# Performance work log

Measured on AMD Instinct MI355X. Metric: run time of the kernel, lower is better.

## Reference

```python
import jax, jax.numpy as jnp
import numpy as np

B, HW, ENC = 64, 14, 2048
L, V, E, D, A = 20, 10000, 512, 512, 512
T = L - 1  # max decode length (one caption forced to length L)


def setup_inputs() -> dict:
    key = jax.random.key(0)
    ks = jax.random.split(key, 16)

    def p(k, shape, s=0.02):
        return jax.random.normal(k, shape, jnp.float32) * s

    cl = jax.random.randint(ks[2], (B,), 5, L + 1).at[0].set(L)
    return {
        "encoder_out": jax.random.normal(ks[0], (B, HW, HW, ENC), jnp.float32),
        "encoded_captions": jax.random.randint(ks[1], (B, L), 0, V),
        "caption_lengths": cl[:, None].astype(jnp.int32),
        "emb": jax.random.uniform(ks[3], (V, E), jnp.float32, -0.1, 0.1),
        "W_ih": p(ks[4], (4 * D, E + ENC)), "b_ih": jnp.zeros((4 * D,), jnp.float32),
        "W_hh": p(ks[5], (4 * D, D)), "b_hh": jnp.zeros((4 * D,), jnp.float32),
        "W_init_h": p(ks[6], (D, ENC)), "b_init_h": jnp.zeros((D,), jnp.float32),
        "W_init_c": p(ks[7], (D, ENC)), "b_init_c": jnp.zeros((D,), jnp.float32),
        "W_fbeta": p(ks[8], (ENC, D)), "b_fbeta": jnp.zeros((ENC,), jnp.float32),
        "W_fc": jax.random.uniform(ks[9], (V, D), jnp.float32, -0.1, 0.1), "b_fc": jnp.zeros((V,), jnp.float32),
        "W_enc_att": p(ks[10], (A, ENC)), "b_enc_att": jnp.zeros((A,), jnp.float32),
        "W_dec_att": p(ks[11], (A, D)), "b_dec_att": jnp.zeros((A,), jnp.float32),
        "W_full_att": p(ks[12], (1, A)), "b_full_att": jnp.zeros((1,), jnp.float32),
    }


def _decode(encoder_out, encoded_captions, caption_lengths, emb,
            W_ih, b_ih, W_hh, b_hh, W_init_h, b_init_h, W_init_c, b_init_c,
            W_fbeta, b_fbeta, W_fc, b_fc, W_enc_att, b_enc_att,
            W_dec_att, b_dec_att, W_full_att, b_full_att):
    b = encoder_out.shape[0]
    enc = encoder_out.reshape(b, -1, encoder_out.shape[-1])  # [B, P, ENC]
    cl = caption_lengths[:, 0]
    sort_ind = jnp.argsort(-cl)  # descending by caption length
    cl = cl[sort_ind]
    enc = enc[sort_ind]
    caps = encoded_captions[sort_ind]
    decode_lengths = cl - 1  # per-sample number of decode steps

    mean_enc = jnp.mean(enc, axis=1)  # [B, ENC]
    h0 = mean_enc @ W_init_h.T + b_init_h
    c0 = mean_enc @ W_init_c.T + b_init_c

    embeddings = emb[caps]  # [B, L, E]
    # encoder-side attention projection is h-independent: precompute once
    att1 = jnp.einsum('bpe,ae->bpa', enc, W_enc_att) + b_enc_att  # [B, P, A]

    xs_emb = jnp.swapaxes(embeddings[:, :T], 0, 1)  # [T, B, E]
    masks = decode_lengths[None, :] > jnp.arange(T)[:, None]  # [T, B]
    # Note: torch slices h[:batch_size_t]; since batch is length-sorted descending,
    # masking inactive rows (freeze state, zero outputs) computes identical values.

    def step(carry, xs):
        h, c = carry
        emb_t, mask = xs
        # Bahdanau soft attention
        att2 = h @ W_dec_att.T + b_dec_att  # [B, A]
        e = jnp.einsum('bpa,a->bp', jnp.tanh(att1 + att2[:, None, :]), W_full_att[0]) + b_full_att[0]
        alpha = jax.nn.softmax(e, axis=1)  # [B, P]
        awe = jnp.einsum('bp,bpe->be', alpha, enc)  # [B, ENC]
        gate = jax.nn.sigmoid(h @ W_fbeta.T + b_fbeta)
        x = jnp.concatenate([emb_t, gate * awe], axis=1)  # [B, E+ENC]
        # LSTMCell (torch gate order: i, f, g, o)
        gates = x @ W_ih.T + b_ih + h @ W_hh.T + b_hh
        i, f, g, o = jnp.split(gates, 4, axis=1)
        c_new = jax.nn.sigmoid(f) * c + jax.nn.sigmoid(i) * jnp.tanh(g)
        h_new = jax.nn.sigmoid(o) * jnp.tanh(c_new)
        preds = h_new @ W_fc.T + b_fc  # dropout = identity in eval
        m = mask[:, None]
        h = jnp.where(m, h_new, h)
        c = jnp.where(m, c_new, c)
        return (h, c), (jnp.where(m, preds, 0.0), jnp.where(m, alpha, 0.0))

    (_, _), (preds, alphas) = jax.lax.scan(step, (h0, c0), (xs_emb, masks))
    predictions = jnp.swapaxes(preds, 0, 1)  # [B, T, V]
    alphas = jnp.swapaxes(alphas, 0, 1)      # [B, T, P]
    return predictions, caps, alphas, sort_ind


def reference(encoder_out, encoded_captions, caption_lengths, emb,
              W_ih, b_ih, W_hh, b_hh, W_init_h, b_init_h, W_init_c, b_init_c,
              W_fbeta, b_fbeta, W_fc, b_fc, W_enc_att, b_enc_att,
              W_dec_att, b_dec_att, W_full_att, b_full_att):
    return _decode(encoder_out, encoded_captions, caption_lengths, emb,
                   W_ih, b_ih, W_hh, b_hh, W_init_h, b_init_h, W_init_c, b_init_c,
                   W_fbeta, b_fbeta, W_fc, b_fc, W_enc_att, b_enc_att,
                   W_dec_att, b_dec_att, W_full_att, b_full_att)
```

## Files before the change

### kernel.cpp

```cpp
#include <hip/hip_runtime.h>
#include <math.h>

#define Bb 64
#define Pp 196
#define ENCd 2048
#define Lc 20
#define Tt 19
#define Vv 10000
#define Ee 512
#define Dd 512
#define Aa 512
#define K2 2560
#define KG 3072
#define G4 2048
#define NPAD 10112

#define OUT_PRED 0ll
#define OUT_CAPS 12160000ll
#define OUT_ALPH 12161280ll
#define OUT_SIND 12399616ll

typedef unsigned short ushort_t;
typedef __attribute__((ext_vector_type(8))) short short8;
typedef __attribute__((ext_vector_type(4))) float f32x4;

#define MFMA16 __builtin_amdgcn_mfma_f32_16x16x32_bf16

__device__ __forceinline__ float b2f(ushort_t u) {
    union { unsigned int i; float f; } x; x.i = ((unsigned int)u) << 16; return x.f;
}
__device__ __forceinline__ ushort_t f2b(float f) {
    union { float f; unsigned int i; } x; x.f = f;
    unsigned int r = x.i + 0x7fffu + ((x.i >> 16) & 1u);
    return (ushort_t)(r >> 16);
}
__device__ __forceinline__ float fsig(float x) { return 1.0f / (1.0f + __expf(-x)); }
__device__ __forceinline__ float ftanh(float x) {
    x = fminf(fmaxf(x, -15.0f), 15.0f);
    float e = __expf(2.0f * x);
    return (e - 1.0f) / (e + 1.0f);
}

__global__ void k_sort(const int* __restrict__ cap_len, const int* __restrict__ caps_in,
                       float* __restrict__ out, int* __restrict__ sind,
                       int* __restrict__ dlen, int* __restrict__ caps_s) {
    __shared__ int cls[Bb];
    int i = threadIdx.x;
    int cl = cap_len[i];
    cls[i] = cl;
    __syncthreads();
    int rank = 0;
    for (int j = 0; j < Bb; ++j) {
        int cj = cls[j];
        rank += (cj > cl) || (cj == cl && j < i);
    }
    sind[rank] = i;
    dlen[rank] = cl - 1;
    out[OUT_SIND + rank] = (float)i;
    for (int l = 0; l < Lc; ++l) {
        int v = caps_in[i * Lc + l];
        caps_s[rank * Lc + l] = v;
        out[OUT_CAPS + rank * Lc + l] = (float)v;
    }
}

__device__ __forceinline__ void cvtseg(const float* __restrict__ src, ushort_t* __restrict__ dst,
                                       int cols, int stride, int off, int bid0, long long quads) {
    long long qid = (long long)bid0 * 256 + threadIdx.x;
    if (qid >= quads) return;
    int c4pr = cols >> 2;
    int r = (int)(qid / c4pr), c4 = (int)(qid % c4pr) << 2;
    float4 v = *(const float4*)&src[(size_t)r * cols + c4];
    ushort4 o; o.x = f2b(v.x); o.y = f2b(v.y); o.z = f2b(v.z); o.w = f2b(v.w);
    *(ushort4*)&dst[(size_t)r * stride + off + c4] = o;
}

__global__ void k_cvtall(const float* Wdec, const float* Wfb, const float* Wih,
                         const float* Whh, const float* Wfc, const float* Wenc_f,
                         const float* Wih0, const float* Wic0,
                         ushort_t* W_ag, ushort_t* W_cat, ushort_t* W_fcb,
                         ushort_t* W_enc, ushort_t* W_hcb) {
    int b = blockIdx.x;
    if      (b < 256)   cvtseg(Wdec,  W_ag,               512,  512,  0,    b,         65536);
    else if (b < 1280)  cvtseg(Wfb,   W_ag + 512 * 512,   512,  512,  0,    b - 256,   262144);
    else if (b < 6400)  cvtseg(Wih,   W_cat,              2560, 3072, 0,    b - 1280,  1310720);
    else if (b < 7424)  cvtseg(Whh,   W_cat,              512,  3072, 2560, b - 6400,  262144);
    else if (b < 12424) cvtseg(Wfc,   W_fcb,              512,  512,  0,    b - 7424,  1280000);
    else if (b < 13448) cvtseg(Wenc_f,W_enc,              2048, 2048, 0,    b - 12424, 262144);
    else if (b < 14472) cvtseg(Wih0,  W_hcb,              2048, 2048, 0,    b - 13448, 262144);
    else                cvtseg(Wic0,  W_hcb + 512 * 2048, 2048, 2048, 0,    b - 14472, 262144);
}

__global__ void k_bias(const float* b_dec, const float* b_fb, const float* b_ihp,
                       const float* b_hhp, const float* b_h, const float* b_c,
                       float* b_ag, float* bsum, float* b_hc) {
    int id = blockIdx.x * 256 + threadIdx.x;
    if (id < 512) b_ag[id] = b_dec[id];
    else if (id < 2560) b_ag[id] = b_fb[id - 512];
    if (id < 2048) bsum[id] = b_ihp[id] + b_hhp[id];
    if (id < 512) b_hc[id] = b_h[id];
    else if (id < 1024) b_hc[id] = b_c[id - 512];
}

__global__ void __launch_bounds__(256) k_enccvt(const float* __restrict__ enc,
                                                const int* __restrict__ sind,
                                                ushort_t* __restrict__ enc_bf) {
    const long long total8 = (long long)Bb * Pp * ENCd / 8;
    for (long long u = (long long)blockIdx.x * 256 + threadIdx.x; u < total8;
         u += (long long)gridDim.x * 256) {
        long long flat = u * 8;
        int r = (int)(flat >> 11);
        int c8 = (int)(flat & 2047);
        int b = r / Pp;
        size_t srow = (size_t)sind[b] * Pp + (r - b * Pp);
        const float* s = enc + srow * ENCd + c8;
        float4 v0 = *(const float4*)s;
        float4 v1 = *(const float4*)(s + 4);
        short8 o;
        o[0] = (short)f2b(v0.x); o[1] = (short)f2b(v0.y); o[2] = (short)f2b(v0.z); o[3] = (short)f2b(v0.w);
        o[4] = (short)f2b(v1.x); o[5] = (short)f2b(v1.y); o[6] = (short)f2b(v1.z); o[7] = (short)f2b(v1.w);
        *(short8*)&enc_bf[(size_t)r * ENCd + c8] = o;
    }
}

__global__ void __launch_bounds__(1024) k_meanenc(const ushort_t* __restrict__ enc_bf,
                                                  ushort_t* __restrict__ mean_bf) {
    int b = blockIdx.x;
    int lane = threadIdx.x & 63, w = threadIdx.x >> 6;
    int cg = w & 3, pg = w >> 2;
    int lc = cg * 512 + lane * 8;
    __shared__ float red[4][2048];
    float acc[8] = {};
    for (int p = pg; p < Pp; p += 4) {
        short8 v = *(const short8*)&enc_bf[((size_t)b * Pp + p) * ENCd + lc];
        #pragma unroll
        for (int j = 0; j < 8; ++j) acc[j] += b2f((ushort_t)v[j]);
    }
    #pragma unroll
    for (int j = 0; j < 8; ++j) red[pg][lc + j] = acc[j];
    __syncthreads();
    int tid = threadIdx.x;
    float2 s = {0.f, 0.f};
    #pragma unroll
    for (int g = 0; g < 4; ++g) {
        float2 v = *(const float2*)&red[g][tid * 2];
        s.x += v.x; s.y += v.y;
    }
    ushort2 o; o.x = f2b(s.x * (1.0f / Pp)); o.y = f2b(s.y * (1.0f / Pp));
    *(ushort2*)&mean_bf[(size_t)b * ENCd + tid * 2] = o;
}

__global__ void __launch_bounds__(256) k_att1(const ushort_t* __restrict__ enc_bf,
                                              const ushort_t* __restrict__ Wenc,
                                              const float* __restrict__ benc,
                                              ushort_t* __restrict__ att1) {
    __shared__ ushort_t As[128 * 64];
    __shared__ ushort_t Bs[128 * 64];
    int tid = threadIdx.x;
    int lane = tid & 63, w = tid >> 6;
    int wr = w >> 1, wc = w & 1;
    int d = blockIdx.x;
    int lid = (d & 7) * 49 + (d >> 3);
    int by = lid >> 2, bx = lid & 3;
    int m0 = by * 128, n0 = bx * 128;
    int r16 = lane & 15;
    f32x4 acc[4][4];
    #pragma unroll
    for (int mf = 0; mf < 4; ++mf)
        #pragma unroll
        for (int nf = 0; nf < 4; ++nf) acc[mf][nf] = (f32x4){0.f, 0.f, 0.f, 0.f};

    int lrow = lane >> 3;
    int lslot = lane & 7;
    for (int k0 = 0; k0 < ENCd; k0 += 64) {
        __syncthreads();
        #pragma unroll
        for (int c = 0; c < 4; ++c) {
            int row = c * 32 + w * 8 + lrow;
            int kg = lslot ^ (row & 7);
            const ushort_t* asrc = enc_bf + (size_t)(m0 + row) * ENCd + k0 + kg * 8;
            const ushort_t* bsrc = Wenc   + (size_t)(n0 + row) * ENCd + k0 + kg * 8;
            __builtin_amdgcn_global_load_lds(
                (const __attribute__((address_space(1))) void*)asrc,
                (__attribute__((address_space(3))) void*)&As[(c * 32 + w * 8) * 64], 16, 0, 0);
            __builtin_amdgcn_global_load_lds(
                (const __attribute__((address_space(1))) void*)bsrc,
                (__attribute__((address_space(3))) void*)&Bs[(c * 32 + w * 8) * 64], 16, 0, 0);
        }
        __syncthreads();
        #pragma unroll
        for (int ks = 0; ks < 2; ++ks) {
            int sl = ks * 4 + (lane >> 4);
            short8 a[4], b[4];
            #pragma unroll
            for (int mf = 0; mf < 4; ++mf) {
                int row = wr * 64 + mf * 16 + r16;
                a[mf] = *(const short8*)&As[row * 64 + ((sl ^ (row & 7)) << 3)];
            }
            #pragma unroll
            for (int nf = 0; nf < 4; ++nf) {
                int row = wc * 64 + nf * 16 + r16;
                b[nf] = *(const short8*)&Bs[row * 64 + ((sl ^ (row & 7)) << 3)];
            }
            #pragma unroll
            for (int mf = 0; mf < 4; ++mf)
                #pragma unroll
                for (int nf = 0; nf < 4; ++nf)
                    acc[mf][nf] = MFMA16(a[mf], b[nf], acc[mf][nf], 0, 0, 0);
        }
    }
    int rj0 = (lane >> 4) << 2;
    #pragma unroll
    for (int mf = 0; mf < 4; ++mf)
        #pragma unroll
        for (int nf = 0; nf < 4; ++nf) {
            int col = n0 + wc * 64 + nf * 16 + r16;
            float bv = benc[col];
            #pragma unroll
            for (int j = 0; j < 4; ++j) {
                int row = m0 + wr * 64 + mf * 16 + rj0 + j;
                att1[(size_t)row * Aa + col] = f2b(acc[mf][nf][j] + bv);
            }
        }
}

__global__ void __launch_bounds__(256) k_h0c0(
        const ushort_t* __restrict__ A, const ushort_t* __restrict__ W,
        const float* __restrict__ bias, ushort_t* __restrict__ hout,
        float* __restrict__ cst) {
    int lane = threadIdx.x & 63, w = threadIdx.x >> 6;
    int r16 = lane & 15, kq = (lane >> 4) << 3;
    int ncol[4];
    #pragma unroll
    for (int tt = 0; tt < 4; ++tt) ncol[tt] = blockIdx.x * 64 + tt * 16 + r16;
    f32x4 acc[4][4];
    #pragma unroll
    for (int mt = 0; mt < 4; ++mt)
        #pragma unroll
        for (int tt = 0; tt < 4; ++tt) acc[mt][tt] = (f32x4){0.f, 0.f, 0.f, 0.f};
    for (int k0 = w * 512; k0 < w * 512 + 512; k0 += 32) {
        short8 a[4];
        #pragma unroll
        for (int mt = 0; mt < 4; ++mt)
            a[mt] = *(const short8*)(A + (size_t)(mt * 16 + r16) * ENCd + k0 + kq);
        #pragma unroll
        for (int tt = 0; tt < 4; ++tt) {
            short8 bw = *(const short8*)&W[(size_t)ncol[tt] * ENCd + k0 + kq];
            #pragma unroll
            for (int mt = 0; mt < 4; ++mt)
                acc[mt][tt] = MFMA16(a[mt], bw, acc[mt][tt], 0, 0, 0);
        }
    }
    __shared__ float red[2][64][68];
    if (w >= 2) {
        float* row = &red[w - 2][lane][0];
        #pragma unroll
        for (int mt = 0; mt < 4; ++mt)
            #pragma unroll
            for (int tt = 0; tt < 4; ++tt) *(f32x4*)&row[(mt * 4 + tt) * 4] = acc[mt][tt];
    }
    __syncthreads();
    if (w < 2) {
        float* row = &red[w][lane][0];
        #pragma unroll
        for (int mt = 0; mt < 4; ++mt)
            #pragma unroll
            for (int tt = 0; tt < 4; ++tt) acc[mt][tt] += *(f32x4*)&row[(mt * 4 + tt) * 4];
    }
    __syncthreads();
    if (w == 1) {
        float* row = &red[0][lane][0];
        #pragma unroll
        for (int mt = 0; mt < 4; ++mt)
            #pragma unroll
            for (int tt = 0; tt < 4; ++tt) *(f32x4*)&row[(mt * 4 + tt) * 4] = acc[mt][tt];
    }
    __syncthreads();
    if (w != 0) return;
    {
        float* row = &red[0][lane][0];
        #pragma unroll
        for (int mt = 0; mt < 4; ++mt)
            #pragma unroll
            for (int tt = 0; tt < 4; ++tt) acc[mt][tt] += *(f32x4*)&row[(mt * 4 + tt) * 4];
    }
    int rj0 = (lane >> 4) << 2;
    #pragma unroll
    for (int mt = 0; mt < 4; ++mt)
        #pragma unroll
        for (int tt = 0; tt < 4; ++tt) {
            int col = ncol[tt];
            float bv = bias[col];
            #pragma unroll
            for (int j = 0; j < 4; ++j) {
                int row = mt * 16 + rj0 + j;
                float v = acc[mt][tt][j] + bv;
                if (col < 512) hout[row * Dd + col] = f2b(v);
                else           cst[row * Dd + (col - 512)] = v;
            }
        }
}

__global__ void __launch_bounds__(256) k_ag(
        const ushort_t* __restrict__ h, const ushort_t* __restrict__ W,
        const float* __restrict__ bias, float* __restrict__ of) {
    int lane = threadIdx.x & 63, w = threadIdx.x >> 6;
    int r16 = lane & 15, kq = (lane >> 4) << 3;
    int col = blockIdx.x * 16 + r16;
    f32x4 acc[4];
    #pragma unroll
    for (int mt = 0; mt < 4; ++mt) acc[mt] = (f32x4){0.f, 0.f, 0.f, 0.f};
    for (int k0 = w * 128; k0 < w * 128 + 128; k0 += 32) {
        short8 bw = *(const short8*)&W[(size_t)col * Dd + k0 + kq];
        #pragma unroll
        for (int mt = 0; mt < 4; ++mt) {
            short8 a = *(const short8*)(h + (size_t)(mt * 16 + r16) * Dd + k0 + kq);
            acc[mt] = MFMA16(a, bw, acc[mt], 0, 0, 0);
        }
    }
    __shared__ float red[2][64][20];
    if (w >= 2) {
        float* rr = &red[w - 2][lane][0];
        #pragma unroll
        for (int mt = 0; mt < 4; ++mt) *(f32x4*)&rr[mt * 4] = acc[mt];
    }
    __syncthreads();
    if (w < 2) {
        float* rr = &red[w][lane][0];
        #pragma unroll
        for (int mt = 0; mt < 4; ++mt) acc[mt] += *(f32x4*)&rr[mt * 4];
    }
    __syncthreads();
    if (w == 1) {
        float* rr = &red[0][lane][0];
        #pragma unroll
        for (int mt = 0; mt < 4; ++mt) *(f32x4*)&rr[mt * 4] = acc[mt];
    }
    __syncthreads();
    if (w != 0) return;
    {
        float* rr = &red[0][lane][0];
        #pragma unroll
        for (int mt = 0; mt < 4; ++mt) acc[mt] += *(f32x4*)&rr[mt * 4];
    }
    int rj0 = (lane >> 4) << 2;
    float bv = bias[col];
    #pragma unroll
    for (int mt = 0; mt < 4; ++mt)
        #pragma unroll
        for (int j = 0; j < 4; ++j) {
            int row = mt * 16 + rj0 + j;
            float v = acc[mt][j] + bv;
            of[(size_t)row * K2 + col] = (col >= 512) ? fsig(v) : v;
        }
}

__global__ void __launch_bounds__(1024) k_esmawe(
        const ushort_t* __restrict__ att1, const float* __restrict__ ag,
        const float* __restrict__ wfull, const float* __restrict__ bfull,
        const ushort_t* __restrict__ enc_bf,
        const float* __restrict__ emb, const int* __restrict__ caps_s,
        ushort_t* __restrict__ x2, float* __restrict__ out,
        const int* __restrict__ dlen, int t) {
    int b = blockIdx.x >> 2, ch = blockIdx.x & 3;
    int tid = threadIdx.x;
    int lane = tid & 63, wv = tid >> 6;
    __shared__ float att2f[512], wfl[512];
    __shared__ float e_sh[200], al_sh[200], sm[4];
    __shared__ float redA[16][512];
    if (tid < 512) att2f[tid] = ag[(size_t)b * K2 + tid];
    else           wfl[tid - 512] = wfull[tid - 512];
    __syncthreads();
    float a2[8], wf8[8];
    #pragma unroll
    for (int j = 0; j < 8; ++j) { a2[j] = att2f[lane * 8 + j]; wf8[j] = wfl[lane * 8 + j]; }
    float bf0 = bfull[0];
    for (int p0 = wv; p0 < Pp; p0 += 32) {
        int p1 = p0 + 16;
        bool has1 = p1 < Pp;
        short8 v0 = *(const short8*)&att1[((size_t)b * Pp + p0) * Aa + lane * 8];
        short8 v1 = has1 ? *(const short8*)&att1[((size_t)b * Pp + p1) * Aa + lane * 8] : v0;
        float s0 = 0.f, s1 = 0.f;
        #pragma unroll
        for (int j = 0; j < 8; ++j) {
            s0 += ftanh(b2f((ushort_t)v0[j]) + a2[j]) * wf8[j];
            s1 += ftanh(b2f((ushort_t)v1[j]) + a2[j]) * wf8[j];
        }
        #pragma unroll
        for (int o = 32; o; o >>= 1) {
            s0 += __shfl_xor(s0, o);
            s1 += __shfl_xor(s1, o);
        }
        if (lane == 0) {
            e_sh[p0] = s0 + bf0;
            if (has1) e_sh[p1] = s1 + bf0;
        }
    }
    __syncthreads();
    if (wv == 0) {
        float v0 = e_sh[lane];
        float v1 = e_sh[lane + 64];
        float v2 = e_sh[lane + 128];
        float v3 = (lane + 192 < Pp) ? e_sh[lane + 192] : -1e30f;
        float m = fmaxf(fmaxf(v0, v1), fmaxf(v2, v3));
        #pragma unroll
        for (int o = 32; o; o >>= 1) m = fmaxf(m, __shfl_xor(m, o));
        float ss = __expf(v0 - m) + __expf(v1 - m) + __expf(v2 - m) + __expf(v3 - m);
        #pragma unroll
        for (int o = 32; o; o >>= 1) ss += __shfl_xor(ss, o);
        if (lane == 0) { sm[0] = m; sm[1] = 1.0f / ss; }
    } else if (ch == 0 && tid >= 512 && tid < 768) {
        int q = tid - 512;
        float2 e2v = *(const float2*)&emb[(size_t)caps_s[b * Lc + t] * Ee + q * 2];
        ushort2 o2; o2.x = f2b(e2v.x); o2.y = f2b(e2v.y);
        *(ushort2*)&x2[(size_t)b * K2 + q * 2] = o2;
    }
    __syncthreads();
    float mx = sm[0], inv = sm[1];
    if (tid < Pp) {
        float al = __expf(e_sh[tid] - mx) * inv;
        al_sh[tid] = al;
        if (ch == 0)
            out[OUT_ALPH + ((long long)b * Tt + t) * Pp + tid] = (t < dlen[b]) ? al : 0.0f;
    }
    __syncthreads();
    {
        int cg = tid & 63, pg = tid >> 6;
        int c0 = cg * 8;
        float acc[8] = {};
        const ushort_t* ep = enc_bf + (size_t)b * Pp * ENCd + ch * 512 + c0;
        for (int p = pg; p < Pp; p += 16) {
            float a = al_sh[p];
            short8 vv = *(const short8*)(ep + (size_t)p * ENCd);
            #pragma unroll
            for (int j = 0; j < 8; ++j) acc[j] += a * b2f((ushort_t)vv[j]);
        }
        *(f32x4*)&redA[pg][c0]     = *(f32x4*)&acc[0];
        *(f32x4*)&redA[pg][c0 + 4] = *(f32x4*)&acc[4];
    }
    __syncthreads();
    if (tid < 512) {
        float s = 0.f;
        #pragma unroll
        for (int g = 0; g < 16; ++g) s += redA[g][tid];
        int col = ch * 512 + tid;
        float gte = ag[(size_t)b * K2 + 512 + col];
        x2[(size_t)b * K2 + Ee + col] = f2b(gte * s);
    }
}

__global__ void __launch_bounds__(512) k_gates(
        const ushort_t* __restrict__ x2, const ushort_t* __restrict__ hin,
        const ushort_t* __restrict__ Wcat, const float* __restrict__ bsum,
        ushort_t* __restrict__ hout, float* __restrict__ cst,
        const int* __restrict__ dlen, int t) {
    int lane = threadIdx.x & 63, w = threadIdx.x >> 6;
    int r16 = lane & 15, kq = (lane >> 4) << 3;
    int m0 = blockIdx.y * 16;
    int d0 = blockIdx.x * 16;
    int row = m0 + r16;
    f32x4 acc[4];
    #pragma unroll
    for (int tt = 0; tt < 4; ++tt) acc[tt] = (f32x4){0.f, 0.f, 0.f, 0.f};
    for (int k0 = w * 384; k0 < w * 384 + 384; k0 += 32) {
        const ushort_t* s = (k0 < K2) ? (x2 + (size_t)row * K2 + k0 + kq)
                                      : (hin + (size_t)row * Dd + (k0 - K2) + kq);
        short8 a = *(const short8*)s;
        #pragma unroll
        for (int tt = 0; tt < 4; ++tt) {
            short8 bw = *(const short8*)&Wcat[(size_t)(d0 + tt * 512 + r16) * KG + k0 + kq];
            acc[tt] = MFMA16(a, bw, acc[tt], 0, 0, 0);
        }
    }
    __shared__ float red[4][64][20];
    for (int s2 = 4; s2; s2 >>= 1) {
        if (w >= s2 && w < 2 * s2) {
            float* rr = &red[w - s2][lane][0];
            #pragma unroll
            for (int tt = 0; tt < 4; ++tt) *(f32x4*)&rr[tt * 4] = acc[tt];
        }
        __syncthreads();
        if (w < s2) {
            float* rr = &red[w][lane][0];
            #pragma unroll
            for (int tt = 0; tt < 4; ++tt) acc[tt] += *(f32x4*)&rr[tt * 4];
        }
        __syncthreads();
    }
    if (w != 0) return;
    int rj0 = (lane >> 4) << 2;
    int d = d0 + r16;
    #pragma unroll
    for (int j = 0; j < 4; ++j) {
        int rw = m0 + rj0 + j;
        ushort_t hb;
        if (t < dlen[rw]) {
            float gi = acc[0][j] + bsum[d];
            float gf = acc[1][j] + bsum[512 + d];
            float gg = acc[2][j] + bsum[1024 + d];
            float go = acc[3][j] + bsum[1536 + d];
            float cv = cst[rw * Dd + d];
            float cn = fsig(gf) * cv + fsig(gi) * ftanh(gg);
            cst[rw * Dd + d] = cn;
            hb = f2b(fsig(go) * ftanh(cn));
        } else {
            hb = hin[rw * Dd + d];
        }
        hout[rw * Dd + d] = hb;
    }
}

__global__ void __launch_bounds__(256) k_preds(
        const ushort_t* __restrict__ hA, const ushort_t* __restrict__ Wfc,
        const float* __restrict__ bfc, const int* __restrict__ dlen,
        float* __restrict__ out) {
    __shared__ ushort_t As[128 * 64];
    __shared__ ushort_t Bs[128 * 64];
    __shared__ float wb[4][16][66];
    int tid = threadIdx.x;
    int lane = tid & 63, w = tid >> 6;
    int wr = w >> 1, wc = w & 1;
    int d = blockIdx.x;
    int x = d & 7, k = d >> 3;
    int lid = (x < 6 ? x * 99 : 594 + (x - 6) * 98) + k;
    int bx = lid / 10, by = lid % 10;
    int m0 = by * 128, n0 = bx * 128;
    int r16 = lane & 15;
    f32x4 acc[4][4];
    #pragma unroll
    for (int mf = 0; mf < 4; ++mf)
        #pragma unroll
        for (int nf = 0; nf < 4; ++nf) acc[mf][nf] = (f32x4){0.f, 0.f, 0.f, 0.f};

    int lrow = lane >> 3;
    int lslot = lane & 7;
    for (int k0 = 0; k0 < Dd; k0 += 64) {
        __syncthreads();
        #pragma unroll
        for (int c = 0; c < 4; ++c) {
            int row = c * 32 + w * 8 + lrow;
            int kg = lslot ^ (row & 7);
            const ushort_t* asrc = hA  + (size_t)(m0 + row) * Dd + k0 + kg * 8;
            const ushort_t* bsrc = Wfc + (size_t)(n0 + row) * Dd + k0 + kg * 8;
            __builtin_amdgcn_global_load_lds(
                (const __attribute__((address_space(1))) void*)asrc,
                (__attribute__((address_space(3))) void*)&As[(c * 32 + w * 8) * 64], 16, 0, 0);
            __builtin_amdgcn_global_load_lds(
                (const __attribute__((address_space(1))) void*)bsrc,
                (__attribute__((address_space(3))) void*)&Bs[(c * 32 + w * 8) * 64], 16, 0, 0);
        }
        __syncthreads();
        #pragma unroll
        for (int ks = 0; ks < 2; ++ks) {
            int sl = ks * 4 + (lane >> 4);
            short8 a[4], b[4];
            #pragma unroll
            for (int mf = 0; mf < 4; ++mf) {
                int row = wr * 64 + mf * 16 + r16;
                a[mf] = *(const short8*)&As[row * 64 + ((sl ^ (row & 7)) << 3)];
            }
            #pragma unroll
            for (int nf = 0; nf < 4; ++nf) {
                int row = wc * 64 + nf * 16 + r16;
                b[nf] = *(const short8*)&Bs[row * 64 + ((sl ^ (row & 7)) << 3)];
            }
            #pragma unroll
            for (int mf = 0; mf < 4; ++mf)
                #pragma unroll
                for (int nf = 0; nf < 4; ++nf)
                    acc[mf][nf] = MFMA16(a[mf], b[nf], acc[mf][nf], 0, 0, 0);
        }
    }
    int rj0 = (lane >> 4) << 2;
    #pragma unroll
    for (int mf = 0; mf < 4; ++mf) {
        #pragma unroll
        for (int nf = 0; nf < 4; ++nf) {
            float bv = bfc[n0 + wc * 64 + nf * 16 + r16];
            #pragma unroll
            for (int j = 0; j < 4; ++j)
                wb[w][rj0 + j][nf * 16 + r16] = acc[mf][nf][j] + bv;
        }
        asm volatile("s_waitcnt lgkmcnt(0)" ::: "memory");
        #pragma unroll
        for (int c = 0; c < 4; ++c) {
            int idx = c * 64 + lane;
            int row16 = idx >> 4, c4 = idx & 15;
            int grow = m0 + wr * 64 + mf * 16 + row16;
            int gcol = n0 + wc * 64 + c4 * 4;
            if (grow < 1216 && gcol < Vv) {
                int ts = grow >> 6, b = grow & 63;
                f32x4 v = *(f32x4*)&wb[w][row16][c4 * 4];
                if (ts >= dlen[b]) v = (f32x4){0.f, 0.f, 0.f, 0.f};
                __builtin_nontemporal_store(v,
                    (f32x4*)&out[OUT_PRED + ((long long)b * Tt + ts) * Vv + gcol]);
            }
        }
        asm volatile("s_waitcnt vmcnt(0)" ::: "memory");
    }
}

extern "C" void kernel_launch(void* const* d_in, const int* in_sizes, int n_in,
                              void* d_out, int out_size, void* d_ws, size_t ws_size,
                              hipStream_t stream) {
    const float* encoder_out      = (const float*)d_in[0];
    const int*   encoded_captions = (const int*)d_in[1];
    const int*   caption_lengths  = (const int*)d_in[2];
    const float* emb       = (const float*)d_in[3];
    const float* W_ih      = (const float*)d_in[4];
    const float* b_ih      = (const float*)d_in[5];
    const float* W_hh      = (const float*)d_in[6];
    const float* b_hh      = (const float*)d_in[7];
    const float* W_init_h  = (const float*)d_in[8];
    const float* b_init_h  = (const float*)d_in[9];
    const float* W_init_c  = (const float*)d_in[10];
    const float* b_init_c  = (const float*)d_in[11];
    const float* W_fbeta   = (const float*)d_in[12];
    const float* b_fbeta   = (const float*)d_in[13];
    const float* W_fc      = (const float*)d_in[14];
    const float* b_fc      = (const float*)d_in[15];
    const float* W_enc_att = (const float*)d_in[16];
    const float* b_enc_att = (const float*)d_in[17];
    const float* W_dec_att = (const float*)d_in[18];
    const float* b_dec_att = (const float*)d_in[19];
    const float* W_full_att = (const float*)d_in[20];
    const float* b_full_att = (const float*)d_in[21];
    float* out = (float*)d_out;

    char* p = (char*)d_ws;
    auto alloc = [&](size_t bytes) { char* r = p; p += (bytes + 255) & ~255ull; return r; };
    int* sind   = (int*)alloc(64 * 4);
    int* dlen   = (int*)alloc(64 * 4);
    int* caps_s = (int*)alloc(Bb * Lc * 4);
    float* c_st  = (float*)alloc(Bb * Dd * 4);
    float* ag    = (float*)alloc((size_t)Bb * K2 * 4);
    float* b_ag  = (float*)alloc(K2 * 4);
    float* bsum  = (float*)alloc(G4 * 4);
    float* b_hc  = (float*)alloc(1024 * 4);
    ushort_t* mean_bf = (ushort_t*)alloc((size_t)Bb * ENCd * 2);
    ushort_t* hball   = (ushort_t*)alloc((size_t)(Tt + 2) * Bb * Dd * 2);
    ushort_t* x2      = (ushort_t*)alloc((size_t)Bb * K2 * 2);
    ushort_t* att1    = (ushort_t*)alloc((size_t)Bb * Pp * Aa * 2);
    ushort_t* W_enc   = (ushort_t*)alloc((size_t)Aa * ENCd * 2);
    ushort_t* W_ag    = (ushort_t*)alloc((size_t)K2 * Dd * 2);
    ushort_t* W_cat   = (ushort_t*)alloc((size_t)G4 * KG * 2);
    ushort_t* W_fcb   = (ushort_t*)alloc((size_t)NPAD * Dd * 2);
    ushort_t* W_hcb   = (ushort_t*)alloc((size_t)1024 * ENCd * 2);
    ushort_t* enc_bf  = (ushort_t*)alloc((size_t)Bb * Pp * ENCd * 2);

    k_sort<<<1, 64, 0, stream>>>(caption_lengths, encoded_captions, out, sind, dlen, caps_s);
    k_cvtall<<<15496, 256, 0, stream>>>(W_dec_att, W_fbeta, W_ih, W_hh, W_fc, W_enc_att,
                                        W_init_h, W_init_c, W_ag, W_cat, W_fcb, W_enc, W_hcb);
    k_bias<<<10, 256, 0, stream>>>(b_dec_att, b_fbeta, b_ih, b_hh, b_init_h, b_init_c,
                                   b_ag, bsum, b_hc);
    k_enccvt<<<2048, 256, 0, stream>>>(encoder_out, sind, enc_bf);
    k_meanenc<<<64, 1024, 0, stream>>>(enc_bf, mean_bf);
    k_h0c0<<<16, 256, 0, stream>>>(mean_bf, W_hcb, b_hc, hball, c_st);
    k_att1<<<392, 256, 0, stream>>>(enc_bf, W_enc, b_enc_att, att1);

    for (int t = 0; t < Tt; ++t) {
        const ushort_t* hcur = hball + (size_t)t * Bb * Dd;
        ushort_t* hnext = hball + (size_t)(t + 1) * Bb * Dd;
        k_ag<<<160, 256, 0, stream>>>(hcur, W_ag, b_ag, ag);
        k_esmawe<<<256, 1024, 0, stream>>>(att1, ag, W_full_att, b_full_att, enc_bf,
            emb, caps_s, x2, out, dlen, t);
        k_gates<<<dim3(32, 4), 512, 0, stream>>>(x2, hcur, W_cat, bsum, hnext, c_st, dlen, t);
    }
    k_preds<<<790, 256, 0, stream>>>(hball + (size_t)Bb * Dd, W_fcb, b_fc, dlen, out);
}
```

Before: 1.152 ms.

## Fuse attention/gate projection of hidden state into attention-weighted encoding kernel

Removes the separate k_ag launch and its global `ag` buffer from each decode step. Each k_esmawe block now computes, with MFMA, the decoder attention projection (512 columns) and its own 512-column slice of the sigmoid gate for its batch row, keeping the results in shared memory. This saves one kernel launch and a global round trip per step. In exchange, each block uses a single broadcast h row in a 16-row MFMA, recomputes the attention projection four times per batch row, and reads about 1 MB of weights per block, which greatly raises weight traffic through the cache.

Result: slower. 1.620 ms (+40.6%).

```diff
diff --git a/kernel.cpp b/kernel.cpp
--- a/kernel.cpp
+++ b/kernel.cpp
@@ -301,62 +301,9 @@
         }
 }
 
-__global__ void __launch_bounds__(256) k_ag(
-        const ushort_t* __restrict__ h, const ushort_t* __restrict__ W,
-        const float* __restrict__ bias, float* __restrict__ of) {
-    int lane = threadIdx.x & 63, w = threadIdx.x >> 6;
-    int r16 = lane & 15, kq = (lane >> 4) << 3;
-    int col = blockIdx.x * 16 + r16;
-    f32x4 acc[4];
-    #pragma unroll
-    for (int mt = 0; mt < 4; ++mt) acc[mt] = (f32x4){0.f, 0.f, 0.f, 0.f};
-    for (int k0 = w * 128; k0 < w * 128 + 128; k0 += 32) {
-        short8 bw = *(const short8*)&W[(size_t)col * Dd + k0 + kq];
-        #pragma unroll
-        for (int mt = 0; mt < 4; ++mt) {
-            short8 a = *(const short8*)(h + (size_t)(mt * 16 + r16) * Dd + k0 + kq);
-            acc[mt] = MFMA16(a, bw, acc[mt], 0, 0, 0);
-        }
-    }
-    __shared__ float red[2][64][20];
-    if (w >= 2) {
-        float* rr = &red[w - 2][lane][0];
-        #pragma unroll
-        for (int mt = 0; mt < 4; ++mt) *(f32x4*)&rr[mt * 4] = acc[mt];
-    }
-    __syncthreads();
-    if (w < 2) {
-        float* rr = &red[w][lane][0];
-        #pragma unroll
-        for (int mt = 0; mt < 4; ++mt) acc[mt] += *(f32x4*)&rr[mt * 4];
-    }
-    __syncthreads();
-    if (w == 1) {
-        float* rr = &red[0][lane][0];
-        #pragma unroll
-        for (int mt = 0; mt < 4; ++mt) *(f32x4*)&rr[mt * 4] = acc[mt];
-    }
-    __syncthreads();
-    if (w != 0) return;
-    {
-        float* rr = &red[0][lane][0];
-        #pragma unroll
-        for (int mt = 0; mt < 4; ++mt) acc[mt] += *(f32x4*)&rr[mt * 4];
-    }
-    int rj0 = (lane >> 4) << 2;
-    float bv = bias[col];
-    #pragma unroll
-    for (int mt = 0; mt < 4; ++mt)
-        #pragma unroll
-        for (int j = 0; j < 4; ++j) {
-            int row = mt * 16 + rj0 + j;
-            float v = acc[mt][j] + bv;
-            of[(size_t)row * K2 + col] = (col >= 512) ? fsig(v) : v;
-        }
-}
-
 __global__ void __launch_bounds__(1024) k_esmawe(
-        const ushort_t* __restrict__ att1, const float* __restrict__ ag,
+        const ushort_t* __restrict__ att1, const ushort_t* __restrict__ hcur,
+        const ushort_t* __restrict__ W_ag, const float* __restrict__ b_ag,
         const float* __restrict__ wfull, const float* __restrict__ bfull,
         const ushort_t* __restrict__ enc_bf,
         const float* __restrict__ emb, const int* __restrict__ caps_s,
@@ -365,11 +312,46 @@
     int b = blockIdx.x >> 2, ch = blockIdx.x & 3;
     int tid = threadIdx.x;
     int lane = tid & 63, wv = tid >> 6;
-    __shared__ float att2f[512], wfl[512];
+    __shared__ float att2f[512], gate_sh[512], wfl[512];
     __shared__ float e_sh[200], al_sh[200], sm[4];
     __shared__ float redA[16][512];
-    if (tid < 512) att2f[tid] = ag[(size_t)b * K2 + tid];
-    else           wfl[tid - 512] = wfull[tid - 512];
+    {
+        const ushort_t* hb = hcur + (size_t)b * Dd;
+        int r16 = lane & 15, kq = (lane >> 4) << 3;
+        f32x4 acc[4];
+        #pragma unroll
+        for (int i = 0; i < 4; ++i) acc[i] = (f32x4){0.f, 0.f, 0.f, 0.f};
+        int t0 = wv * 4;
+        const ushort_t* wbase[4];
+        #pragma unroll
+        for (int i = 0; i < 4; ++i) {
+            int tile = t0 + i;
+            int wrow = (tile < 32) ? tile * 16 : 512 + ch * 512 + (tile - 32) * 16;
+            wbase[i] = W_ag + (size_t)(wrow + r16) * Dd + kq;
+        }
+        for (int k0 = 0; k0 < Dd; k0 += 32) {
+            short8 a = *(const short8*)(hb + k0 + kq);
+            #pragma unroll
+            for (int i = 0; i < 4; ++i) {
+                short8 bw = *(const short8*)(wbase[i] + k0);
+                acc[i] = MFMA16(a, bw, acc[i], 0, 0, 0);
+            }
+        }
+        if (lane < 16) {
+            #pragma unroll
+            for (int i = 0; i < 4; ++i) {
+                int tile = t0 + i;
+                if (tile < 32) {
+                    int col = tile * 16 + lane;
+                    att2f[col] = acc[i][0] + b_ag[col];
+                } else {
+                    int col = (tile - 32) * 16 + lane;
+                    gate_sh[col] = fsig(acc[i][0] + b_ag[512 + ch * 512 + col]);
+                }
+            }
+        }
+    }
+    if (tid >= 512) wfl[tid - 512] = wfull[tid - 512];
     __syncthreads();
     float a2[8], wf8[8];
     #pragma unroll
@@ -444,8 +426,7 @@
         #pragma unroll
         for (int g = 0; g < 16; ++g) s += redA[g][tid];
         int col = ch * 512 + tid;
-        float gte = ag[(size_t)b * K2 + 512 + col];
-        x2[(size_t)b * K2 + Ee + col] = f2b(gte * s);
+        x2[(size_t)b * K2 + Ee + col] = f2b(gate_sh[tid] * s);
     }
 }
 
@@ -633,7 +614,6 @@
     int* dlen   = (int*)alloc(64 * 4);
     int* caps_s = (int*)alloc(Bb * Lc * 4);
     float* c_st  = (float*)alloc(Bb * Dd * 4);
-    float* ag    = (float*)alloc((size_t)Bb * K2 * 4);
     float* b_ag  = (float*)alloc(K2 * 4);
     float* bsum  = (float*)alloc(G4 * 4);
     float* b_hc  = (float*)alloc(1024 * 4);
@@ -661,9 +641,8 @@
     for (int t = 0; t < Tt; ++t) {
         const ushort_t* hcur = hball + (size_t)t * Bb * Dd;
         ushort_t* hnext = hball + (size_t)(t + 1) * Bb * Dd;
-        k_ag<<<160, 256, 0, stream>>>(hcur, W_ag, b_ag, ag);
-        k_esmawe<<<256, 1024, 0, stream>>>(att1, ag, W_full_att, b_full_att, enc_bf,
-            emb, caps_s, x2, out, dlen, t);
+        k_esmawe<<<256, 1024, 0, stream>>>(att1, hcur, W_ag, b_ag, W_full_att, b_full_att,
+            enc_bf, emb, caps_s, x2, out, dlen, t);
         k_gates<<<dim3(32, 4), 512, 0, stream>>>(x2, hcur, W_cat, bsum, hnext, c_st, dlen, t);
     }
     k_preds<<<790, 256, 0, stream>>>(hball + (size_t)Bb * Dd, W_fcb, b_fc, dlen, out);
```
